# Kernel optimization log

Hardware: AMD Instinct MI355X
Metric: run time of the kernel (lower is better)

## Reference

```python
import jax, jax.numpy as jnp
import numpy as np
import math

H = 128
HEADS = 2
NEG = -float(1 << 32)
BN_EPS = 1e-5
LN_EPS = 1e-5


def _bn_eval(x, g, b):
    # BatchNorm1d in eval mode with running_mean=0, running_var=1
    return g * (x / jnp.sqrt(1.0 + BN_EPS)) + b


def _ln(x, g, b):
    mu = x.mean(-1, keepdims=True)
    var = ((x - mu) ** 2).mean(-1, keepdims=True)
    return g * (x - mu) / jnp.sqrt(var + LN_EPS) + b


def _multi_embed(tables, idx):
    # tables [F,V,H], idx [N,F] -> sum_f tables[f, idx[:,f]]  (ogb Atom/BondEncoder)
    F = tables.shape[0]
    return tables[jnp.arange(F)[None, :], idx].sum(axis=1)


def _gin_graph(x, edge_attr, edge_index, batch, num_graphs, atom_emb, bond_emb, eps, w1, b1, g1, be1, w2, b2, g2, be2):
    h = _multi_embed(atom_emb, x)  # [N,H]
    tgt, src = edge_index[0], edge_index[1]
    L = eps.shape[0]
    for l in range(L):
        e = _multi_embed(bond_emb[l], edge_attr)  # [E,H]
        msg = jax.nn.relu(h[src] + e)
        agg = jax.ops.segment_sum(msg, tgt, num_segments=h.shape[0])
        z = (1.0 + eps[l]) * h + agg
        z = jax.nn.relu(_bn_eval(z @ w1[l] + b1[l], g1[l], be1[l])) @ w2[l] + b2[l]
        h = _bn_eval(z, g2[l], be2[l])
        if l != L - 1:
            h = jax.nn.relu(h)  # dropout is identity in eval mode
    s = jax.ops.segment_sum(h, batch, num_segments=num_graphs)
    c = jax.ops.segment_sum(jnp.ones_like(h), batch, num_segments=num_graphs)
    return s / (c + 1e-9)  # mean pooling per graph


def _sab(X, wq, bq, wk, bk, wv, bv, wo, bo, l1g, l1b, l2g, l2b):
    # MAB(X, X) with HEADS heads, use_ln=True. X: [B,S,H]
    B, S, _ = X.shape
    dh = H // HEADS

    def split(T):  # torch split(last)+cat(dim0): head-major [HEADS*B, S, dh]
        return T.reshape(B, S, HEADS, dh).transpose(2, 0, 1, 3).reshape(HEADS * B, S, dh)

    Qs, Ks, Vs = split(X @ wq + bq), split(X @ wk + bk), split(X @ wv + bv)
    A = jax.nn.softmax(jnp.einsum('bqd,bkd->bqk', Qs, Ks) / math.sqrt(dh), axis=-1)
    O = Qs + jnp.einsum('bqk,bkd->bqd', A, Vs)
    O = O.reshape(HEADS, B, S, dh).transpose(1, 2, 0, 3).reshape(B, S, H)
    O = _ln(O, l1g, l1b)
    O = _ln(O @ wo + bo, l2g, l2b)
    return O


def setup_inputs() -> dict:
    key = jax.random.key(0)
    ks = iter(jax.random.split(key, 64))
    nk = lambda: next(ks)
    V, L = 64, 4
    NS, ES = 60000, 140000
    NM, EM = 150000, 350000
    S, M, D, B = 492, 600, 200, 64
    f32 = jnp.float32
    w = lambda *shp: jax.random.normal(nk(), shp, f32) * 0.05
    inp = {}
    inp['atom_emb'] = w(2, 9, V, H)
    inp['bond_emb'] = w(2, L, 3, V, H)
    inp['gin_eps'] = jnp.zeros((2, L), f32)
    inp['gin_w1'] = w(2, L, H, 2 * H); inp['gin_b1'] = jnp.zeros((2, L, 2 * H), f32)
    inp['gin_bn1_g'] = jnp.ones((2, L, 2 * H), f32); inp['gin_bn1_b'] = jnp.zeros((2, L, 2 * H), f32)
    inp['gin_w2'] = w(2, L, 2 * H, H); inp['gin_b2'] = jnp.zeros((2, L, H), f32)
    inp['gin_bn2_g'] = jnp.ones((2, L, H), f32); inp['gin_bn2_b'] = jnp.zeros((2, L, H), f32)
    for nm in ['sab_wq', 'sab_wk', 'sab_wv', 'sab_wo']:
        inp[nm] = w(H, H)
    for nm in ['sab_bq', 'sab_bk', 'sab_bv', 'sab_bo', 'sab_ln1_b', 'sab_ln2_b']:
        inp[nm] = jnp.zeros((H,), f32)
    inp['sab_ln1_g'] = jnp.ones((H,), f32); inp['sab_ln2_g'] = jnp.ones((H,), f32)
    inp['agg_wq'] = w(H, H); inp['agg_bq'] = jnp.zeros((H,), f32)
    inp['agg_wk'] = w(H, H); inp['agg_bk'] = jnp.zeros((H,), f32)
    inp['score_w1'] = w(H, H // 2); inp['score_b1'] = jnp.zeros((H // 2,), f32)
    inp['score_w2'] = w(H // 2, 1); inp['score_b2'] = jnp.zeros((1,), f32)
    inp['patient_emb'] = jax.random.uniform(nk(), (B, S), f32)
    inp['average_projection'] = jax.random.uniform(nk(), (D, M), f32) / M
    inp['sub_x'] = jax.random.randint(nk(), (NS, 9), 0, V)
    inp['sub_edge_attr'] = jax.random.randint(nk(), (ES, 3), 0, V)
    inp['sub_edge_index'] = jax.random.randint(nk(), (2, ES), 0, NS)
    inp['sub_batch'] = jax.random.randint(nk(), (NS,), 0, S)
    inp['mol_x'] = jax.random.randint(nk(), (NM, 9), 0, V)
    inp['mol_edge_attr'] = jax.random.randint(nk(), (EM, 3), 0, V)
    inp['mol_edge_index'] = jax.random.randint(nk(), (2, EM), 0, NM)
    inp['mol_batch'] = jax.random.randint(nk(), (NM,), 0, M)
    mask = jax.random.bernoulli(nk(), 0.3, (D, S))
    inp['mask'] = mask.at[:, 0].set(False)
    inp['num_sub'] = S
    inp['num_mol'] = M
    return inp


def reference(atom_emb, bond_emb, gin_eps, gin_w1, gin_b1, gin_bn1_g, gin_bn1_b, gin_w2, gin_b2, gin_bn2_g, gin_bn2_b, sab_wq, sab_bq, sab_wk, sab_bk, sab_wv, sab_bv, sab_wo, sab_bo, sab_ln1_g, sab_ln1_b, sab_ln2_g, sab_ln2_b, agg_wq, agg_bq, agg_wk, agg_bk, score_w1, score_b1, score_w2, score_b2, patient_emb, average_projection, sub_x, sub_edge_attr, sub_edge_index, sub_batch, mol_x, mol_edge_attr, mol_edge_index, mol_batch, mask, num_sub, num_mol):
    # substructure encoder (GINGraph #0) + SAB interaction
    sub = _gin_graph(sub_x, sub_edge_attr, sub_edge_index, sub_batch, num_sub, atom_emb[0], bond_emb[0], gin_eps[0], gin_w1[0], gin_b1[0], gin_bn1_g[0], gin_bn1_b[0], gin_w2[0], gin_b2[0], gin_bn2_g[0], gin_bn2_b[0])
    sub = _sab(sub[None], sab_wq, sab_bq, sab_wk, sab_bk, sab_wv, sab_bv, sab_wo, sab_bo, sab_ln1_g, sab_ln1_b, sab_ln2_g, sab_ln2_b)[0]  # [S,H]
    # molecule encoder (GINGraph #1) + drug-level averaging
    mol = _gin_graph(mol_x, mol_edge_attr, mol_edge_index, mol_batch, num_mol, atom_emb[1], bond_emb[1], gin_eps[1], gin_w1[1], gin_b1[1], gin_bn1_g[1], gin_bn1_b[1], gin_w2[1], gin_b2[1], gin_bn2_g[1], gin_bn2_b[1])
    mol_emb = average_projection @ mol  # [D,H]
    # AttnAgg: masked attention, per-patient reweighting via diag(fix_feat)
    Q = mol_emb @ agg_wq + agg_bq
    K = sub @ agg_wk + agg_bk
    attn = (Q @ K.T) / math.sqrt(H)
    attn = jax.nn.softmax(jnp.where(mask, NEG, attn), axis=-1)  # [D,S]
    agg = jnp.einsum('ds,bs,sh->bdh', attn, patient_emb, sub)  # [B,D,H]
    logits = (jax.nn.relu(agg @ score_w1 + score_b1) @ score_w2 + score_b2)[..., 0]
    return jax.nn.sigmoid(logits)  # y_prob [B,D]
```

## Files before the change

### kernel.cpp

```cpp
#include <hip/hip_runtime.h>


typedef short short8 __attribute__((ext_vector_type(8)));
typedef unsigned short us8 __attribute__((ext_vector_type(8)));
typedef float f32x4 __attribute__((ext_vector_type(4)));
typedef unsigned short us4 __attribute__((ext_vector_type(4)));

#define BN_RSQ 0.9999950000374997f
#define LN_EPS 1e-5f
#define NEGBIG -4294967296.0f

__device__ __forceinline__ unsigned short f2bf(float x) {
  union { float f; unsigned int u; } v; v.f = x;
  unsigned int r = v.u + 0x7fffu + ((v.u >> 16) & 1u);
  return (unsigned short)(r >> 16);
}
__device__ __forceinline__ float bf2f(unsigned short x) {
  union { unsigned int u; float f; } v; v.u = ((unsigned int)x) << 16;
  return v.f;
}

__global__ void prep_weights(const float* __restrict__ w1, const float* __restrict__ w2,
                             unsigned short* __restrict__ w1t, unsigned short* __restrict__ w2t) {
  int i = blockIdx.x * 256 + threadIdx.x;
  if (i >= 262144) return;
  int gl = i >> 15;
  int k1 = (i >> 8) & 127, c1 = i & 255;
  w1t[(gl << 15) + c1 * 128 + k1] = f2bf(w1[i]);
  int k2 = (i >> 7) & 255, c2 = i & 127;
  w2t[(gl << 15) + c2 * 256 + k2] = f2bf(w2[i]);
}

__global__ void prep_bond(const float* __restrict__ in, unsigned short* __restrict__ out, int n) {
  int i = blockIdx.x * 256 + threadIdx.x;
  if (i < n) out[i] = f2bf(in[i]);
}

__global__ __launch_bounds__(256) void mask_detect(const unsigned char* __restrict__ m,
                                                   int* __restrict__ flags, int nbytes) {
  __shared__ int lf[2];
  if (threadIdx.x == 0) { lf[0] = 0; lf[1] = 0; }
  __syncthreads();
  int f0 = 0, f1 = 0;
  for (int i = blockIdx.x * 256 + threadIdx.x; i < nbytes; i += gridDim.x * 256) {
    if (m[i]) { if ((i & 3) == 0) f0 = 1; else f1 = 1; }
  }
  if (f0) atomicOr(&lf[0], 1);
  if (f1) atomicOr(&lf[1], 1);
  __syncthreads();
  if (threadIdx.x == 0) {
    if (lf[0]) atomicOr(flags, 1);
    if (lf[1]) atomicOr(flags + 1, 1);
  }
}

__global__ void build_count(const int* __restrict__ ei_m, int Em,
                            const int* __restrict__ ei_s, int Es,
                            const int* __restrict__ bm, int Nm,
                            const int* __restrict__ bs, int Ns,
                            int* __restrict__ deg_e, int* __restrict__ deg_n,
                            int M, int NmR) {
  int i = blockIdx.x * 256 + threadIdx.x;
  if (i < Em) { atomicAdd(&deg_e[ei_m[i]], 1); return; }
  i -= Em;
  if (i < Es) { atomicAdd(&deg_e[NmR + ei_s[i]], 1); return; }
  i -= Es;
  if (i < Nm) { atomicAdd(&deg_n[bm[i]], 1); return; }
  i -= Nm;
  if (i < Ns) { atomicAdd(&deg_n[M + bs[i]], 1); }
}

__global__ __launch_bounds__(256) void scan_block(const int* __restrict__ cnt, int n,
                                                  int* __restrict__ excl, int* __restrict__ bsum) {
  int gid = blockIdx.x * 256 + threadIdx.x;
  int lane = threadIdx.x & 63, w = threadIdx.x >> 6;
  int v = (gid < n) ? cnt[gid] : 0;
  int x = v;
#pragma unroll
  for (int off = 1; off < 64; off <<= 1) {
    int y = __shfl_up(x, off, 64);
    if (lane >= off) x += y;
  }
  __shared__ int wt[4];
  if (lane == 63) wt[w] = x;
  __syncthreads();
  int add = 0;
  for (int i = 0; i < w; i++) add += wt[i];
  x += add;
  if (gid < n) excl[gid] = x - v;
  if (threadIdx.x == 255) bsum[blockIdx.x] = x;
}

__global__ __launch_bounds__(1024) void scan_top(int* __restrict__ bsum, int n) {
  int t = threadIdx.x;
  int lane = t & 63, w = t >> 6;
  int v = (t < n) ? bsum[t] : 0;
  int x = v;
#pragma unroll
  for (int off = 1; off < 64; off <<= 1) {
    int y = __shfl_up(x, off, 64);
    if (lane >= off) x += y;
  }
  __shared__ int wt[16];
  if (lane == 63) wt[w] = x;
  __syncthreads();
  int add = 0;
  for (int i = 0; i < w; i++) add += wt[i];
  x += add;
  if (t < n) bsum[t] = x - v;
}

__global__ void finalize_rowptr(const int* __restrict__ excl, const int* __restrict__ bsum,
                                int n, int total, int* __restrict__ rowptr) {
  int i = blockIdx.x * 256 + threadIdx.x;
  if (i < n) rowptr[i] = excl[i] + bsum[i >> 8];
  if (i == n) rowptr[n] = total;
}

__global__ void scatter_edges(const int* __restrict__ ei_m, const int* __restrict__ ea_m, int Em,
                              const int* __restrict__ ei_s, const int* __restrict__ ea_s, int Es, int NmR,
                              const int* __restrict__ rowptr_e,
                              int* __restrict__ cur_e, int4* __restrict__ epool) {
  int i = blockIdx.x * 256 + threadIdx.x;
  int g, src, a0, a1, a2;
  if (i < Em) {
    g = ei_m[i]; src = ei_m[Em + i];
    a0 = ea_m[i * 3]; a1 = ea_m[i * 3 + 1]; a2 = ea_m[i * 3 + 2];
  } else {
    int j = i - Em; if (j >= Es) return;
    g = NmR + ei_s[j]; src = NmR + ei_s[Es + j];
    a0 = ea_s[j * 3]; a1 = ea_s[j * 3 + 1]; a2 = ea_s[j * 3 + 2];
  }
  int slot = rowptr_e[g] + atomicAdd(&cur_e[g], 1);
  int p0 = a0 * 128, p1 = (64 + a1) * 128, p2 = (128 + a2) * 128;
  epool[slot] = make_int4(src * 128, 0, p0 | (p1 << 16), p2);
}

__global__ void scatter_nodes(const int* __restrict__ bm, int Nm,
                              const int* __restrict__ bs, int Ns, int M, int NmR,
                              const int* __restrict__ rowptr_n,
                              int* __restrict__ cur_n, int* __restrict__ npool) {
  int i = blockIdx.x * 256 + threadIdx.x;
  int g, node;
  if (i < Nm) { g = bm[i]; node = i; }
  else { int j = i - Nm; if (j >= Ns) return; g = M + bs[j]; node = NmR + j; }
  int slot = rowptr_n[g] + atomicAdd(&cur_n[g], 1);
  npool[slot] = node;
}

__global__ void embed_nodes(const int* __restrict__ x, const float* __restrict__ table,
                            unsigned short* __restrict__ h, int N) {
  int i = blockIdx.x * 256 + threadIdx.x;
  if (i >= N * 128) return;
  int n = i >> 7, c = i & 127;
  float s = 0.f;
#pragma unroll
  for (int f = 0; f < 9; f++) {
    int v = x[n * 9 + f];
    s += table[(f * 64 + v) * 128 + c];
  }
  h[i] = f2bf(s);
}

__global__ __launch_bounds__(256, 4) void gin_fused3(
    const unsigned short* __restrict__ hin, unsigned short* __restrict__ hout,
    const float* __restrict__ eps_all, int l, int NmR,
    const unsigned short* __restrict__ bt16,
    const int4* __restrict__ epool, const int* __restrict__ rowptr_e,
    const unsigned short* __restrict__ w1t_a, const float* __restrict__ b1_a,
    const float* __restrict__ g1_a, const float* __restrict__ be1_a,
    const unsigned short* __restrict__ w2t_a, const float* __restrict__ b2_a,
    const float* __restrict__ g2_a, const float* __restrict__ be2_a) {
  __shared__ __align__(16) unsigned char smem[38144];
  unsigned short* z1s = (unsigned short*)smem;
  unsigned short* zs  = (unsigned short*)(smem + 20736);
  int t = threadIdx.x;
  int r0 = blockIdx.x * 64;
  int g = (r0 < NmR) ? 1 : 0;
  int gl = g * 4 + l;
  const unsigned short* bt = bt16 + (size_t)gl * 3 * 64 * 128;
  const unsigned short* w1t = w1t_a + (size_t)gl * 32768;
  const unsigned short* w2t = w2t_a + (size_t)gl * 32768;
  const float* b1 = b1_a + gl * 256;
  const float* g1 = g1_a + gl * 256;
  const float* be1 = be1_a + gl * 256;
  const float* b2 = b2_a + gl * 128;
  const float* g2 = g2_a + gl * 128;
  const float* be2 = be2_a + gl * 128;
  float eps1 = 1.0f + eps_all[gl];
  int do_relu = (l != 3);

#pragma unroll
  for (int p = 0; p < 2; p++) {
    int lr = p * 32 + (t >> 3);
    int n = r0 + lr;
    int cb = (t & 7) * 16;
    float acc[16];
    {
      const unsigned short* hr = hin + (size_t)n * 128 + cb;
      us8 v0 = *(const us8*)hr, v1 = *(const us8*)(hr + 8);
#pragma unroll
      for (int k = 0; k < 8; k++) {
        acc[k]     = eps1 * bf2f(v0[k]);
        acc[8 + k] = eps1 * bf2f(v1[k]);
      }
    }
    int e0 = rowptr_e[n], e1 = rowptr_e[n + 1];
    for (int e = e0; e < e1; e++) {
      int4 rec = epool[e];
      const unsigned short* hs = hin + rec.x + cb;
      const unsigned short* q0 = bt + (rec.z & 0xffff) + cb;
      const unsigned short* q1 = bt + (((unsigned)rec.z) >> 16) + cb;
      const unsigned short* q2 = bt + rec.w + cb;
      us8 a0 = *(const us8*)hs, a1 = *(const us8*)(hs + 8);
      us8 b0 = *(const us8*)q0, b1v = *(const us8*)(q0 + 8);
      us8 c0 = *(const us8*)q1, c1 = *(const us8*)(q1 + 8);
      us8 d0 = *(const us8*)q2, d1 = *(const us8*)(q2 + 8);
#pragma unroll
      for (int k = 0; k < 8; k++) {
        acc[k]     += fmaxf(bf2f(a0[k]) + bf2f(b0[k]) + bf2f(c0[k]) + bf2f(d0[k]), 0.f);
        acc[8 + k] += fmaxf(bf2f(a1[k]) + bf2f(b1v[k]) + bf2f(c1[k]) + bf2f(d1[k]), 0.f);
      }
    }
    unsigned short ob[16];
#pragma unroll
    for (int k = 0; k < 16; k++) ob[k] = f2bf(acc[k]);
    unsigned short* zr = zs + lr * 136 + cb;
    *(us8*)zr = *(const us8*)&ob[0];
    *(us8*)(zr + 8) = *(const us8*)&ob[8];
  }
  __syncthreads();

  int lane = t & 63, wave = t >> 6;
  int quad = lane >> 4, l16 = lane & 15;
  {
    short8 bw[4][4];
    int cb = wave * 64;
#pragma unroll
    for (int nt = 0; nt < 4; nt++) {
      const unsigned short* p = w1t + (cb + nt * 16 + l16) * 128 + quad * 8;
#pragma unroll
      for (int kc = 0; kc < 4; kc++) bw[nt][kc] = *(const short8*)(p + kc * 32);
    }
    for (int mt = 0; mt < 4; mt++) {
      short8 af[4];
      const unsigned short* zrow = zs + (mt * 16 + l16) * 136 + quad * 8;
#pragma unroll
      for (int kc = 0; kc < 4; kc++)
        af[kc] = *(const short8*)(zrow + kc * 32);
#pragma unroll
      for (int nt = 0; nt < 4; nt++) {
        f32x4 acc = {0.f, 0.f, 0.f, 0.f};
#pragma unroll
        for (int kc = 0; kc < 4; kc++)
          acc = __builtin_amdgcn_mfma_f32_16x16x32_bf16(af[kc], bw[nt][kc], acc, 0, 0, 0);
        int c = cb + nt * 16 + l16;
        float sc = g1[c] * BN_RSQ, sh = be1[c], bb = b1[c];
#pragma unroll
        for (int reg = 0; reg < 4; reg++) {
          int r = mt * 16 + quad * 4 + reg;
          float y = (acc[reg] + bb) * sc + sh;
          z1s[r * 264 + c] = f2bf(fmaxf(y, 0.f));
        }
      }
      __syncthreads();
    }
  }
  {
    short8 bw[2][8];
    int cb = wave * 32;
#pragma unroll
    for (int nt = 0; nt < 2; nt++) {
      const unsigned short* p = w2t + (cb + nt * 16 + l16) * 256 + quad * 8;
#pragma unroll
      for (int kc = 0; kc < 8; kc++) bw[nt][kc] = *(const short8*)(p + kc * 32);
    }
    for (int mt = 0; mt < 4; mt++) {
      short8 af[8];
      const unsigned short* zrow = z1s + (mt * 16 + l16) * 264 + quad * 8;
#pragma unroll
      for (int kc = 0; kc < 8; kc++)
        af[kc] = *(const short8*)(zrow + kc * 32);
      __syncthreads();
#pragma unroll
      for (int nt = 0; nt < 2; nt++) {
        f32x4 acc = {0.f, 0.f, 0.f, 0.f};
#pragma unroll
        for (int kc = 0; kc < 8; kc++)
          acc = __builtin_amdgcn_mfma_f32_16x16x32_bf16(af[kc], bw[nt][kc], acc, 0, 0, 0);
        int c = cb + nt * 16 + l16;
        float sc = g2[c] * BN_RSQ, sh = be2[c], bb = b2[c];
#pragma unroll
        for (int reg = 0; reg < 4; reg++) {
          int r = mt * 16 + quad * 4 + reg;
          float y = (acc[reg] + bb) * sc + sh;
          if (do_relu) y = fmaxf(y, 0.f);
          z1s[r * 264 + c] = f2bf(y);
        }
      }
    }
  }
  __syncthreads();
  for (int i = t; i < 1024; i += 256) {
    int r = i >> 4, c8 = (i & 15) * 8;
    us8 v = *(const us8*)(z1s + r * 264 + c8);
    *(us8*)(hout + (size_t)(r0 + r) * 128 + c8) = v;
  }
}

__global__ __launch_bounds__(128) void pool_csr(const unsigned short* __restrict__ h,
                                                const int* __restrict__ npool,
                                                const int* __restrict__ rowptr_n,
                                                float* __restrict__ pooled, int nseg) {
  int m = blockIdx.x;
  if (m >= nseg) return;
  int st = rowptr_n[m];
  int e = rowptr_n[m + 1];
  int len = e - st;
  int c = threadIdx.x;
  float s = 0.f;
  int i = st;
  for (; i + 3 < e; i += 4) {
    int n0 = npool[i], n1 = npool[i + 1], n2 = npool[i + 2], n3 = npool[i + 3];
    float v0 = bf2f(h[(size_t)n0 * 128 + c]);
    float v1 = bf2f(h[(size_t)n1 * 128 + c]);
    float v2 = bf2f(h[(size_t)n2 * 128 + c]);
    float v3 = bf2f(h[(size_t)n3 * 128 + c]);
    s += (v0 + v1) + (v2 + v3);
  }
  for (; i < e; i++) s += bf2f(h[(size_t)npool[i] * 128 + c]);
  pooled[m * 128 + c] = s / ((float)len + 1e-9f);
}

__global__ __launch_bounds__(256) void gemm_tile(const float* __restrict__ A, const float* __restrict__ W,
                                                 const float* __restrict__ bias, float* __restrict__ C,
                                                 int K) {
  __shared__ float As[608];
  __shared__ float red[128];
  int r = blockIdx.x;
  int t = threadIdx.x;
  for (int i = t; i < K; i += 256) As[i] = A[(size_t)r * K + i];
  __syncthreads();
  int c = t & 127, half = t >> 7;
  int Kh = K >> 1;
  int k0 = half * Kh, k1 = k0 + Kh;
  float acc = 0.f;
#pragma unroll 8
  for (int k = k0; k < k1; k++) acc = fmaf(As[k], W[(size_t)k * 128 + c], acc);
  if (half) red[c] = acc;
  __syncthreads();
  if (!half) {
    float v = acc + red[c] + (bias ? bias[c] : 0.f);
    C[(size_t)r * 128 + c] = v;
  }
}

__global__ __launch_bounds__(256) void gemm_qkv(const float* __restrict__ A,
                                                const float* __restrict__ W0, const float* __restrict__ bi0, float* __restrict__ C0,
                                                const float* __restrict__ W1, const float* __restrict__ bi1, float* __restrict__ C1,
                                                const float* __restrict__ W2, const float* __restrict__ bi2, float* __restrict__ C2) {
  __shared__ float As[128];
  __shared__ float red[128];
  int r = blockIdx.x, which = blockIdx.y;
  const float* W = (which == 0) ? W0 : (which == 1) ? W1 : W2;
  const float* bias = (which == 0) ? bi0 : (which == 1) ? bi1 : bi2;
  float* C = (which == 0) ? C0 : (which == 1) ? C1 : C2;
  int t = threadIdx.x;
  if (t < 128) As[t] = A[(size_t)r * 128 + t];
  __syncthreads();
  int c = t & 127, half = t >> 7;
  int k0 = half * 64, k1 = k0 + 64;
  float acc = 0.f;
#pragma unroll 8
  for (int k = k0; k < k1; k++) acc = fmaf(As[k], W[(size_t)k * 128 + c], acc);
  if (half) red[c] = acc;
  __syncthreads();
  if (!half) C[(size_t)r * 128 + c] = acc + red[c] + bias[c];
}

__global__ __launch_bounds__(256) void sab_attn(const float* __restrict__ Q, const float* __restrict__ K,
                                                const float* __restrict__ V, float* __restrict__ O, int S) {
  int q = blockIdx.x, hd = blockIdx.y;
  int t = threadIdx.x;
  __shared__ float sc[512];
  __shared__ float red[8];
  __shared__ float pacc[4][64];
  const float* qrow = Q + q * 128 + hd * 64;
  for (int k = t; k < 512; k += 256) {
    float d = -1e30f;
    if (k < S) {
      const float* krow = K + k * 128 + hd * 64;
      d = 0.f;
#pragma unroll
      for (int j = 0; j < 64; j += 4) {
        float4 a = *(const float4*)(qrow + j);
        float4 b = *(const float4*)(krow + j);
        d += a.x * b.x + a.y * b.y + a.z * b.z + a.w * b.w;
      }
      d *= 0.125f;
    }
    sc[k] = d;
  }
  __syncthreads();
  float m = fmaxf(sc[t], sc[t + 256]);
  for (int off = 32; off; off >>= 1) m = fmaxf(m, __shfl_down(m, off));
  if ((t & 63) == 0) red[t >> 6] = m;
  __syncthreads();
  m = fmaxf(fmaxf(red[0], red[1]), fmaxf(red[2], red[3]));
  float p0 = __expf(sc[t] - m), p1 = __expf(sc[t + 256] - m);
  sc[t] = p0; sc[t + 256] = p1;
  float s = p0 + p1;
  for (int off = 32; off; off >>= 1) s += __shfl_down(s, off);
  if ((t & 63) == 0) red[4 + (t >> 6)] = s;
  __syncthreads();
  float inv = 1.f / (red[4] + red[5] + red[6] + red[7]);
  int d = t & 63, part = t >> 6;
  float acc = 0.f;
  for (int k = part; k < S; k += 4) acc += sc[k] * V[k * 128 + hd * 64 + d];
  pacc[part][d] = acc;
  __syncthreads();
  if (part == 0) {
    float o = (pacc[0][d] + pacc[1][d] + pacc[2][d] + pacc[3][d]) * inv;
    O[q * 128 + hd * 64 + d] = qrow[d] + o;
  }
}

__global__ __launch_bounds__(128) void ln_rows(const float* __restrict__ in, float* __restrict__ out,
                                               const float* __restrict__ g, const float* __restrict__ b) {
  int r = blockIdx.x, t = threadIdx.x;
  __shared__ float red[4];
  float x = in[r * 128 + t];
  float s = x;
  for (int off = 32; off; off >>= 1) s += __shfl_down(s, off);
  if ((t & 63) == 0) red[t >> 6] = s;
  __syncthreads();
  float mu = (red[0] + red[1]) * (1.f / 128.f);
  float dd = x - mu;
  float v = dd * dd;
  for (int off = 32; off; off >>= 1) v += __shfl_down(v, off);
  if ((t & 63) == 0) red[2 + (t >> 6)] = v;
  __syncthreads();
  float var = (red[2] + red[3]) * (1.f / 128.f);
  out[r * 128 + t] = g[t] * dd * rsqrtf(var + LN_EPS) + b[t];
}

__global__ __launch_bounds__(256) void agg_attn(const float* __restrict__ Q, const float* __restrict__ Kt,
                                                const void* __restrict__ mask, const int* __restrict__ flags,
                                                float* __restrict__ attn, int D, int S) {
  int d = blockIdx.x, t = threadIdx.x;
  __shared__ float sc[512];
  __shared__ float red[8];
  int layout = (flags[1] == 0) ? 0 : (flags[0] ? 1 : 2);
  const float* qrow = Q + d * 128;
  for (int s = t; s < 512; s += 256) {
    float v = NEGBIG;
    if (s < S) {
      int mi = d * S + s;
      bool msk;
      if (layout == 0)      msk = ((const int*)mask)[mi] != 0;
      else if (layout == 1) msk = ((const unsigned char*)mask)[mi] != 0;
      else                  msk = ((const float*)mask)[mi] != 0.f;
      if (!msk) {
        float dd = 0.f;
        const float* krow = Kt + s * 128;
#pragma unroll
        for (int j = 0; j < 128; j += 4) {
          float4 a = *(const float4*)(qrow + j);
          float4 b = *(const float4*)(krow + j);
          dd += a.x * b.x + a.y * b.y + a.z * b.z + a.w * b.w;
        }
        v = dd * 0.08838834764831845f;
      }
    }
    sc[s] = v;
  }
  __syncthreads();
  float m = fmaxf(sc[t], sc[t + 256]);
  for (int off = 32; off; off >>= 1) m = fmaxf(m, __shfl_down(m, off));
  if ((t & 63) == 0) red[t >> 6] = m;
  __syncthreads();
  m = fmaxf(fmaxf(red[0], red[1]), fmaxf(red[2], red[3]));
  float p0 = __expf(sc[t] - m), p1 = __expf(sc[t + 256] - m);
  float s2 = p0 + p1;
  for (int off = 32; off; off >>= 1) s2 += __shfl_down(s2, off);
  if ((t & 63) == 0) red[4 + (t >> 6)] = s2;
  __syncthreads();
  float inv = 1.f / (red[4] + red[5] + red[6] + red[7]);
  attn[d * S + t] = p0 * inv;
  if (t + 256 < S) attn[d * S + t + 256] = p1 * inv;
}

__global__ void prep_subT(const float* __restrict__ subf, unsigned short* __restrict__ subT, int S) {
  int i = blockIdx.x * 256 + threadIdx.x;
  if (i >= 128 * 512) return;
  int hh = i >> 9, k = i & 511;
  subT[i] = (k < S) ? f2bf(subf[k * 128 + hh]) : (unsigned short)0;
}

__global__ __launch_bounds__(256) void agg_mfma(const float* __restrict__ attn, const float* __restrict__ pat,
                                                const unsigned short* __restrict__ subT,
                                                float* __restrict__ aggT, int D, int S) {
  int d = blockIdx.x, t = threadIdx.x;
  __shared__ unsigned short As[64][40];
  int lane = t & 63, wave = t >> 6;
  int quad = lane >> 4, l16 = lane & 15;
  f32x4 acc[8];
#pragma unroll
  for (int nt = 0; nt < 8; nt++) acc[nt] = (f32x4){0.f, 0.f, 0.f, 0.f};
  const float* arow = attn + d * S;
  int srow = t >> 2, skb = (t & 3) * 8;
  for (int c = 0; c < 16; c++) {
    int s0 = c * 32;
    __syncthreads();
    unsigned short v[8];
#pragma unroll
    for (int j = 0; j < 8; j++) {
      int s = s0 + skb + j;
      float x = (s < S) ? arow[s] * pat[srow * S + s] : 0.f;
      v[j] = f2bf(x);
    }
    *(us4*)&As[srow][skb]     = *(us4*)&v[0];
    *(us4*)&As[srow][skb + 4] = *(us4*)&v[4];
    __syncthreads();
    short8 af = *(const short8*)&As[16 * wave + l16][quad * 8];
#pragma unroll
    for (int nt = 0; nt < 8; nt++) {
      short8 bf = *(const short8*)(subT + (nt * 16 + l16) * 512 + s0 + quad * 8);
      acc[nt] = __builtin_amdgcn_mfma_f32_16x16x32_bf16(af, bf, acc[nt], 0, 0, 0);
    }
  }
#pragma unroll
  for (int nt = 0; nt < 8; nt++) {
    int hh = nt * 16 + l16;
#pragma unroll
    for (int reg = 0; reg < 4; reg++) {
      int b = 16 * wave + quad * 4 + reg;
      aggT[((size_t)(b * D + d)) * 128 + hh] = acc[nt][reg];
    }
  }
}

__global__ __launch_bounds__(256) void score_head(const float* __restrict__ aggT,
                                                  const float* __restrict__ w1, const float* __restrict__ b1,
                                                  const float* __restrict__ w2, const float* __restrict__ b2,
                                                  float* __restrict__ out, int total) {
  int i = blockIdx.x * 4 + (threadIdx.x >> 6);
  int j = threadIdx.x & 63;
  if (i >= total) return;
  const float* av = aggT + (size_t)i * 128;
  float acc = b1[j];
#pragma unroll 8
  for (int k = 0; k < 128; k++) acc = fmaf(av[k], w1[k * 64 + j], acc);
  acc = fmaxf(acc, 0.f) * w2[j];
  for (int off = 32; off; off >>= 1) acc += __shfl_down(acc, off);
  if (j == 0) {
    float x = acc + b2[0];
    out[i] = 1.f / (1.f + __expf(-x));
  }
}

extern "C" void kernel_launch(void* const* d_in, const int* in_sizes, int n_in,
                              void* d_out, int out_size, void* d_ws, size_t ws_size,
                              hipStream_t stream) {
  const float* atom_emb = (const float*)d_in[0];
  const float* bond_emb = (const float*)d_in[1];
  const float* gin_eps  = (const float*)d_in[2];
  const float* gin_w1   = (const float*)d_in[3];
  const float* gin_b1   = (const float*)d_in[4];
  const float* bn1g     = (const float*)d_in[5];
  const float* bn1b     = (const float*)d_in[6];
  const float* gin_w2   = (const float*)d_in[7];
  const float* gin_b2   = (const float*)d_in[8];
  const float* bn2g     = (const float*)d_in[9];
  const float* bn2b     = (const float*)d_in[10];
  const float* sab_wq = (const float*)d_in[11];
  const float* sab_wk = (const float*)d_in[12];
  const float* sab_wv = (const float*)d_in[13];
  const float* sab_wo = (const float*)d_in[14];
  const float* sab_bq = (const float*)d_in[15];
  const float* sab_bk = (const float*)d_in[16];
  const float* sab_bv = (const float*)d_in[17];
  const float* sab_bo = (const float*)d_in[18];
  const float* ln1b = (const float*)d_in[19];
  const float* ln2b = (const float*)d_in[20];
  const float* ln1g = (const float*)d_in[21];
  const float* ln2g = (const float*)d_in[22];
  const float* agg_wq = (const float*)d_in[23];
  const float* agg_bq = (const float*)d_in[24];
  const float* agg_wk = (const float*)d_in[25];
  const float* agg_bk = (const float*)d_in[26];
  const float* score_w1 = (const float*)d_in[27];
  const float* score_b1 = (const float*)d_in[28];
  const float* score_w2 = (const float*)d_in[29];
  const float* score_b2 = (const float*)d_in[30];
  const float* patient  = (const float*)d_in[31];
  const float* avgproj  = (const float*)d_in[32];
  const int* sub_x     = (const int*)d_in[33];
  const int* sub_ea    = (const int*)d_in[34];
  const int* sub_ei    = (const int*)d_in[35];
  const int* sub_batch = (const int*)d_in[36];
  const int* mol_x     = (const int*)d_in[37];
  const int* mol_ea    = (const int*)d_in[38];
  const int* mol_ei    = (const int*)d_in[39];
  const int* mol_batch = (const int*)d_in[40];
  const void* mask     = d_in[41];

  const int Ns = in_sizes[33] / 9, Es = in_sizes[34] / 3;
  const int Nm = in_sizes[37] / 9, Em = in_sizes[38] / 3;
  const int S = 492, M = 600, D = 200, B = 64;
  const int NmR = (Nm + 63) & ~63;
  const int NsR = (Ns + 63) & ~63;
  const int NTOT = NmR + NsR;
  const int NSEG = M + S;
  const int ETOT = Em + Es;
  const int BONDE = 2 * 4 * 3 * 64 * 128;

  char* Wp = (char*)d_ws;
  size_t off = 0;
  auto alloc = [&](size_t bytes) -> void* {
    void* p = Wp + off;
    off = (off + bytes + 255) & ~(size_t)255;
    return p;
  };
  unsigned short* h0 = (unsigned short*)alloc((size_t)NTOT * 128 * 2);
  unsigned short* h1 = (unsigned short*)alloc((size_t)NTOT * 128 * 2);
  unsigned short* w1t = (unsigned short*)alloc(262144 * 2);
  unsigned short* w2t = (unsigned short*)alloc(262144 * 2);
  unsigned short* bt16 = (unsigned short*)alloc((size_t)BONDE * 2);
  int4* epool  = (int4*)alloc((size_t)ETOT * 16);
  int*  npool  = (int*)alloc((size_t)(Nm + Ns) * 4);
  int*  excl_e = (int*)alloc((size_t)NTOT * 4);
  int*  bsum_e = (int*)alloc(1024 * 4);
  int*  excl_n = (int*)alloc((size_t)NSEG * 4);
  int*  bsum_n = (int*)alloc(1024 * 4);
  int*  rowptr_e = (int*)alloc((size_t)(NTOT + 1) * 4);
  int*  rowptr_n = (int*)alloc((size_t)(NSEG + 1) * 4);
  char* zstart = Wp + off;
  int*  deg_e  = (int*)alloc((size_t)NTOT * 4);
  int*  deg_n  = (int*)alloc((size_t)NSEG * 4);
  int*  cur_e  = (int*)alloc((size_t)NTOT * 4);
  int*  cur_n  = (int*)alloc((size_t)NSEG * 4);
  int*  flags  = (int*)alloc(8);
  size_t zsize = (size_t)((Wp + off) - zstart);
  float* pooled_all = (float*)alloc((size_t)NSEG * 128 * 4);
  float* pooled_mol = pooled_all;
  float* pooled_sub = pooled_all + (size_t)M * 128;
  float* Qb   = (float*)alloc((size_t)S * 128 * 4);
  float* Kb   = (float*)alloc((size_t)S * 128 * 4);
  float* Vb   = (float*)alloc((size_t)S * 128 * 4);
  float* Ob   = (float*)alloc((size_t)S * 128 * 4);
  float* O2b  = (float*)alloc((size_t)S * 128 * 4);
  float* subf = (float*)alloc((size_t)S * 128 * 4);
  unsigned short* subT = (unsigned short*)alloc((size_t)128 * 512 * 2);
  float* mol_embb = (float*)alloc((size_t)D * 128 * 4);
  float* aggQb = (float*)alloc((size_t)D * 128 * 4);
  float* aggKb = (float*)alloc((size_t)S * 128 * 4);
  float* attnb = (float*)alloc((size_t)D * S * 4);
  float* aggTb = (float*)alloc((size_t)B * D * 128 * 4);
  (void)ws_size; (void)n_in; (void)out_size;

  hipMemsetAsync(zstart, 0, zsize, stream);
  prep_weights<<<1024, 256, 0, stream>>>(gin_w1, gin_w2, w1t, w2t);
  prep_bond<<<(BONDE + 255) / 256, 256, 0, stream>>>(bond_emb, bt16, BONDE);
  mask_detect<<<64, 256, 0, stream>>>((const unsigned char*)mask, flags, D * S);

  int total_cnt = Em + Es + Nm + Ns;
  build_count<<<(total_cnt + 255) / 256, 256, 0, stream>>>(
      mol_ei, Em, sub_ei, Es, mol_batch, Nm, sub_batch, Ns, deg_e, deg_n, M, NmR);
  int nb_e = (NTOT + 255) / 256;
  int nb_n = (NSEG + 255) / 256;
  scan_block<<<nb_e, 256, 0, stream>>>(deg_e, NTOT, excl_e, bsum_e);
  scan_top<<<1, 1024, 0, stream>>>(bsum_e, nb_e);
  scan_block<<<nb_n, 256, 0, stream>>>(deg_n, NSEG, excl_n, bsum_n);
  scan_top<<<1, 1024, 0, stream>>>(bsum_n, nb_n);
  finalize_rowptr<<<(NTOT + 256) / 256 + 1, 256, 0, stream>>>(excl_e, bsum_e, NTOT, ETOT, rowptr_e);
  finalize_rowptr<<<(NSEG + 256) / 256 + 1, 256, 0, stream>>>(excl_n, bsum_n, NSEG, Nm + Ns, rowptr_n);
  scatter_edges<<<(ETOT + 255) / 256, 256, 0, stream>>>(
      mol_ei, mol_ea, Em, sub_ei, sub_ea, Es, NmR, rowptr_e, cur_e, epool);
  scatter_nodes<<<(Nm + Ns + 255) / 256, 256, 0, stream>>>(
      mol_batch, Nm, sub_batch, Ns, M, NmR, rowptr_n, cur_n, npool);

  embed_nodes<<<(Nm * 128 + 255) / 256, 256, 0, stream>>>(
      mol_x, atom_emb + (size_t)1 * 9 * 64 * 128, h0, Nm);
  embed_nodes<<<(Ns * 128 + 255) / 256, 256, 0, stream>>>(
      sub_x, atom_emb + (size_t)0 * 9 * 64 * 128, h0 + (size_t)NmR * 128, Ns);
  unsigned short* hin = h0; unsigned short* hout = h1;
  for (int l = 0; l < 4; l++) {
    gin_fused3<<<NTOT / 64, 256, 0, stream>>>(
        hin, hout, gin_eps, l, NmR, bt16, epool, rowptr_e,
        w1t, gin_b1, bn1g, bn1b, w2t, gin_b2, bn2g, bn2b);
    unsigned short* tmp = hin; hin = hout; hout = tmp;
  }
  pool_csr<<<NSEG, 128, 0, stream>>>(hin, npool, rowptr_n, pooled_all, NSEG);

  gemm_qkv<<<dim3(S, 3), 256, 0, stream>>>(pooled_sub,
                                           sab_wq, sab_bq, Qb,
                                           sab_wk, sab_bk, Kb,
                                           sab_wv, sab_bv, Vb);
  sab_attn<<<dim3(S, 2), 256, 0, stream>>>(Qb, Kb, Vb, Ob, S);
  ln_rows<<<S, 128, 0, stream>>>(Ob, Ob, ln1g, ln1b);
  gemm_tile<<<S, 256, 0, stream>>>(Ob, sab_wo, sab_bo, O2b, 128);
  ln_rows<<<S, 128, 0, stream>>>(O2b, subf, ln2g, ln2b);
  prep_subT<<<(128 * 512 + 255) / 256, 256, 0, stream>>>(subf, subT, S);

  gemm_tile<<<D, 256, 0, stream>>>(avgproj, pooled_mol, (const float*)nullptr, mol_embb, 600);

  gemm_tile<<<D, 256, 0, stream>>>(mol_embb, agg_wq, agg_bq, aggQb, 128);
  gemm_tile<<<S, 256, 0, stream>>>(subf, agg_wk, agg_bk, aggKb, 128);
  agg_attn<<<D, 256, 0, stream>>>(aggQb, aggKb, mask, flags, attnb, D, S);
  agg_mfma<<<D, 256, 0, stream>>>(attnb, patient, subT, aggTb, D, S);
  score_head<<<(B * D + 3) / 4, 256, 0, stream>>>(aggTb, score_w1, score_b1, score_w2, score_b2,
                                                  (float*)d_out, B * D);
}
```

Before: 1.045 ms.

## Merge small preprocessing kernels and fuse Wo GEMM with LayerNorm

Several small setup launches are merged into combined kernels: weight, bond and mask prep, the two prefix scans, the row-pointer finalisation, the edge and node scatters, the two embeddings, and the two attention Q/K projections. The Wo projection is fused with the second LayerNorm, which removes an intermediate buffer. The GIN aggregation loop also unpacks bf16 pairs straight from 32-bit words instead of per-element conversion. The goal is less launch overhead and fewer global round trips, at the cost of branchier combined kernels.

```diff
diff --git a/kernel.cpp b/kernel.cpp
--- a/kernel.cpp
+++ b/kernel.cpp
@@ -5,6 +5,7 @@
 typedef unsigned short us8 __attribute__((ext_vector_type(8)));
 typedef float f32x4 __attribute__((ext_vector_type(4)));
 typedef unsigned short us4 __attribute__((ext_vector_type(4)));
+typedef unsigned int u32;
 
 #define BN_RSQ 0.9999950000374997f
 #define LN_EPS 1e-5f
@@ -20,29 +21,31 @@
   return v.f;
 }
 
-__global__ void prep_weights(const float* __restrict__ w1, const float* __restrict__ w2,
-                             unsigned short* __restrict__ w1t, unsigned short* __restrict__ w2t) {
-  int i = blockIdx.x * 256 + threadIdx.x;
-  if (i >= 262144) return;
-  int gl = i >> 15;
-  int k1 = (i >> 8) & 127, c1 = i & 255;
-  w1t[(gl << 15) + c1 * 128 + k1] = f2bf(w1[i]);
-  int k2 = (i >> 7) & 255, c2 = i & 127;
-  w2t[(gl << 15) + c2 * 256 + k2] = f2bf(w2[i]);
-}
-
-__global__ void prep_bond(const float* __restrict__ in, unsigned short* __restrict__ out, int n) {
-  int i = blockIdx.x * 256 + threadIdx.x;
-  if (i < n) out[i] = f2bf(in[i]);
-}
-
-__global__ __launch_bounds__(256) void mask_detect(const unsigned char* __restrict__ m,
-                                                   int* __restrict__ flags, int nbytes) {
+__global__ __launch_bounds__(256) void prep_all(
+    const float* __restrict__ w1, const float* __restrict__ w2,
+    unsigned short* __restrict__ w1t, unsigned short* __restrict__ w2t,
+    const float* __restrict__ bond, unsigned short* __restrict__ bt16, int bonde,
+    const unsigned char* __restrict__ m, int* __restrict__ flags, int maskn) {
   __shared__ int lf[2];
+  int b = blockIdx.x;
+  if (b < 1024) {
+    int i = b * 256 + threadIdx.x;
+    int gl = i >> 15;
+    int k1 = (i >> 8) & 127, c1 = i & 255;
+    w1t[(gl << 15) + c1 * 128 + k1] = f2bf(w1[i]);
+    int k2 = (i >> 7) & 255, c2 = i & 127;
+    w2t[(gl << 15) + c2 * 256 + k2] = f2bf(w2[i]);
+    return;
+  }
+  if (b < 1792) {
+    int i = (b - 1024) * 256 + threadIdx.x;
+    if (i < bonde) bt16[i] = f2bf(bond[i]);
+    return;
+  }
   if (threadIdx.x == 0) { lf[0] = 0; lf[1] = 0; }
   __syncthreads();
   int f0 = 0, f1 = 0;
-  for (int i = blockIdx.x * 256 + threadIdx.x; i < nbytes; i += gridDim.x * 256) {
+  for (int i = (b - 1792) * 256 + threadIdx.x; i < maskn; i += 64 * 256) {
     if (m[i]) { if ((i & 3) == 0) f0 = 1; else f1 = 1; }
   }
   if (f0) atomicOr(&lf[0], 1);
@@ -70,9 +73,13 @@
   if (i < Ns) { atomicAdd(&deg_n[M + bs[i]], 1); }
 }
 
-__global__ __launch_bounds__(256) void scan_block(const int* __restrict__ cnt, int n,
-                                                  int* __restrict__ excl, int* __restrict__ bsum) {
-  int gid = blockIdx.x * 256 + threadIdx.x;
+__global__ __launch_bounds__(256) void scan_block2(
+    const int* __restrict__ cntE, int nE, int* __restrict__ exclE, int* __restrict__ bsumE, int nbE,
+    const int* __restrict__ cntN, int nN, int* __restrict__ exclN, int* __restrict__ bsumN) {
+  const int* cnt; int n; int* excl; int* bsum; int blk;
+  if (blockIdx.x < (unsigned)nbE) { cnt = cntE; n = nE; excl = exclE; bsum = bsumE; blk = blockIdx.x; }
+  else { cnt = cntN; n = nN; excl = exclN; bsum = bsumN; blk = blockIdx.x - nbE; }
+  int gid = blk * 256 + threadIdx.x;
   int lane = threadIdx.x & 63, w = threadIdx.x >> 6;
   int v = (gid < n) ? cnt[gid] : 0;
   int x = v;
@@ -88,10 +95,13 @@
   for (int i = 0; i < w; i++) add += wt[i];
   x += add;
   if (gid < n) excl[gid] = x - v;
-  if (threadIdx.x == 255) bsum[blockIdx.x] = x;
-}
-
-__global__ __launch_bounds__(1024) void scan_top(int* __restrict__ bsum, int n) {
+  if (threadIdx.x == 255) bsum[blk] = x;
+}
+
+__global__ __launch_bounds__(1024) void scan_top2(int* __restrict__ bsumE, int nE,
+                                                  int* __restrict__ bsumN, int nN) {
+  int* bsum = blockIdx.x ? bsumN : bsumE;
+  int n = blockIdx.x ? nN : nE;
   int t = threadIdx.x;
   int lane = t & 63, w = t >> 6;
   int v = (t < n) ? bsum[t] : 0;
@@ -110,56 +120,71 @@
   if (t < n) bsum[t] = x - v;
 }
 
-__global__ void finalize_rowptr(const int* __restrict__ excl, const int* __restrict__ bsum,
-                                int n, int total, int* __restrict__ rowptr) {
+__global__ void finalize2(const int* __restrict__ exclE, const int* __restrict__ bsumE,
+                          int nE, int totE, int* __restrict__ rowE,
+                          const int* __restrict__ exclN, const int* __restrict__ bsumN,
+                          int nN, int totN, int* __restrict__ rowN) {
   int i = blockIdx.x * 256 + threadIdx.x;
-  if (i < n) rowptr[i] = excl[i] + bsum[i >> 8];
-  if (i == n) rowptr[n] = total;
-}
-
-__global__ void scatter_edges(const int* __restrict__ ei_m, const int* __restrict__ ea_m, int Em,
-                              const int* __restrict__ ei_s, const int* __restrict__ ea_s, int Es, int NmR,
-                              const int* __restrict__ rowptr_e,
-                              int* __restrict__ cur_e, int4* __restrict__ epool) {
+  if (i <= nE) {
+    rowE[i] = (i < nE) ? (exclE[i] + bsumE[i >> 8]) : totE;
+    return;
+  }
+  int j = i - nE - 1;
+  if (j <= nN) rowN[j] = (j < nN) ? (exclN[j] + bsumN[j >> 8]) : totN;
+}
+
+__global__ void scatter2(const int* __restrict__ ei_m, const int* __restrict__ ea_m, int Em,
+                         const int* __restrict__ ei_s, const int* __restrict__ ea_s, int Es, int NmR,
+                         const int* __restrict__ rowptr_e, int* __restrict__ cur_e,
+                         int4* __restrict__ epool,
+                         const int* __restrict__ bm, int Nm,
+                         const int* __restrict__ bs, int Ns, int M,
+                         const int* __restrict__ rowptr_n, int* __restrict__ cur_n,
+                         int* __restrict__ npool) {
   int i = blockIdx.x * 256 + threadIdx.x;
-  int g, src, a0, a1, a2;
-  if (i < Em) {
-    g = ei_m[i]; src = ei_m[Em + i];
-    a0 = ea_m[i * 3]; a1 = ea_m[i * 3 + 1]; a2 = ea_m[i * 3 + 2];
-  } else {
-    int j = i - Em; if (j >= Es) return;
-    g = NmR + ei_s[j]; src = NmR + ei_s[Es + j];
-    a0 = ea_s[j * 3]; a1 = ea_s[j * 3 + 1]; a2 = ea_s[j * 3 + 2];
-  }
-  int slot = rowptr_e[g] + atomicAdd(&cur_e[g], 1);
-  int p0 = a0 * 128, p1 = (64 + a1) * 128, p2 = (128 + a2) * 128;
-  epool[slot] = make_int4(src * 128, 0, p0 | (p1 << 16), p2);
-}
-
-__global__ void scatter_nodes(const int* __restrict__ bm, int Nm,
-                              const int* __restrict__ bs, int Ns, int M, int NmR,
-                              const int* __restrict__ rowptr_n,
-                              int* __restrict__ cur_n, int* __restrict__ npool) {
-  int i = blockIdx.x * 256 + threadIdx.x;
+  if (i < Em + Es) {
+    int g, src, a0, a1, a2;
+    if (i < Em) {
+      g = ei_m[i]; src = ei_m[Em + i];
+      a0 = ea_m[i * 3]; a1 = ea_m[i * 3 + 1]; a2 = ea_m[i * 3 + 2];
+    } else {
+      int j = i - Em;
+      g = NmR + ei_s[j]; src = NmR + ei_s[Es + j];
+      a0 = ea_s[j * 3]; a1 = ea_s[j * 3 + 1]; a2 = ea_s[j * 3 + 2];
+    }
+    int slot = rowptr_e[g] + atomicAdd(&cur_e[g], 1);
+    int p0 = a0 * 128, p1 = (64 + a1) * 128, p2 = (128 + a2) * 128;
+    epool[slot] = make_int4(src * 128, 0, p0 | (p1 << 16), p2);
+    return;
+  }
+  int k = i - (Em + Es);
+  if (k >= Nm + Ns) return;
   int g, node;
-  if (i < Nm) { g = bm[i]; node = i; }
-  else { int j = i - Nm; if (j >= Ns) return; g = M + bs[j]; node = NmR + j; }
+  if (k < Nm) { g = bm[k]; node = k; }
+  else { int j = k - Nm; g = M + bs[j]; node = NmR + j; }
   int slot = rowptr_n[g] + atomicAdd(&cur_n[g], 1);
   npool[slot] = node;
 }
 
-__global__ void embed_nodes(const int* __restrict__ x, const float* __restrict__ table,
-                            unsigned short* __restrict__ h, int N) {
+__global__ void embed2(const int* __restrict__ xm, const int* __restrict__ xs,
+                       const float* __restrict__ atab, int Nm, int Ns, int NmR,
+                       unsigned short* __restrict__ h) {
   int i = blockIdx.x * 256 + threadIdx.x;
-  if (i >= N * 128) return;
-  int n = i >> 7, c = i & 127;
+  const int* x; const float* table; int n, c, outn;
+  if (i < Nm * 128) {
+    n = i >> 7; c = i & 127; x = xm; table = atab + (size_t)9 * 64 * 128; outn = n;
+  } else {
+    int j = i - Nm * 128;
+    if (j >= Ns * 128) return;
+    n = j >> 7; c = j & 127; x = xs; table = atab; outn = NmR + n;
+  }
   float s = 0.f;
 #pragma unroll
   for (int f = 0; f < 9; f++) {
     int v = x[n * 9 + f];
     s += table[(f * 64 + v) * 128 + c];
   }
-  h[i] = f2bf(s);
+  h[(size_t)outn * 128 + c] = f2bf(s);
 }
 
 __global__ __launch_bounds__(256, 4) void gin_fused3(
@@ -195,39 +220,50 @@
     int lr = p * 32 + (t >> 3);
     int n = r0 + lr;
     int cb = (t & 7) * 16;
-    float acc[16];
+    float lo[8], hi[8];
     {
-      const unsigned short* hr = hin + (size_t)n * 128 + cb;
-      us8 v0 = *(const us8*)hr, v1 = *(const us8*)(hr + 8);
-#pragma unroll
-      for (int k = 0; k < 8; k++) {
-        acc[k]     = eps1 * bf2f(v0[k]);
-        acc[8 + k] = eps1 * bf2f(v1[k]);
+      const u32* hr = (const u32*)(hin + (size_t)n * 128 + cb);
+      uint4 h0v = *(const uint4*)hr;
+      uint4 h1v = *(const uint4*)(hr + 4);
+      u32 hd[8] = {h0v.x, h0v.y, h0v.z, h0v.w, h1v.x, h1v.y, h1v.z, h1v.w};
+#pragma unroll
+      for (int j = 0; j < 8; j++) {
+        lo[j] = eps1 * __uint_as_float(hd[j] << 16);
+        hi[j] = eps1 * __uint_as_float(hd[j] & 0xffff0000u);
       }
     }
     int e0 = rowptr_e[n], e1 = rowptr_e[n + 1];
     for (int e = e0; e < e1; e++) {
       int4 rec = epool[e];
-      const unsigned short* hs = hin + rec.x + cb;
-      const unsigned short* q0 = bt + (rec.z & 0xffff) + cb;
-      const unsigned short* q1 = bt + (((unsigned)rec.z) >> 16) + cb;
-      const unsigned short* q2 = bt + rec.w + cb;
-      us8 a0 = *(const us8*)hs, a1 = *(const us8*)(hs + 8);
-      us8 b0 = *(const us8*)q0, b1v = *(const us8*)(q0 + 8);
-      us8 c0 = *(const us8*)q1, c1 = *(const us8*)(q1 + 8);
-      us8 d0 = *(const us8*)q2, d1 = *(const us8*)(q2 + 8);
-#pragma unroll
-      for (int k = 0; k < 8; k++) {
-        acc[k]     += fmaxf(bf2f(a0[k]) + bf2f(b0[k]) + bf2f(c0[k]) + bf2f(d0[k]), 0.f);
-        acc[8 + k] += fmaxf(bf2f(a1[k]) + bf2f(b1v[k]) + bf2f(c1[k]) + bf2f(d1[k]), 0.f);
+      const u32* hs = (const u32*)(hin + rec.x + cb);
+      const u32* q0 = (const u32*)(bt + (rec.z & 0xffff) + cb);
+      const u32* q1 = (const u32*)(bt + (((unsigned)rec.z) >> 16) + cb);
+      const u32* q2 = (const u32*)(bt + rec.w + cb);
+      uint4 A0 = *(const uint4*)hs, A1 = *(const uint4*)(hs + 4);
+      uint4 B0 = *(const uint4*)q0, B1 = *(const uint4*)(q0 + 4);
+      uint4 C0 = *(const uint4*)q1, C1 = *(const uint4*)(q1 + 4);
+      uint4 D0 = *(const uint4*)q2, D1 = *(const uint4*)(q2 + 4);
+      u32 ad[8] = {A0.x, A0.y, A0.z, A0.w, A1.x, A1.y, A1.z, A1.w};
+      u32 bd[8] = {B0.x, B0.y, B0.z, B0.w, B1.x, B1.y, B1.z, B1.w};
+      u32 cd[8] = {C0.x, C0.y, C0.z, C0.w, C1.x, C1.y, C1.z, C1.w};
+      u32 dd[8] = {D0.x, D0.y, D0.z, D0.w, D1.x, D1.y, D1.z, D1.w};
+#pragma unroll
+      for (int j = 0; j < 8; j++) {
+        float sl = __uint_as_float(ad[j] << 16) + __uint_as_float(bd[j] << 16)
+                 + __uint_as_float(cd[j] << 16) + __uint_as_float(dd[j] << 16);
+        float sh = __uint_as_float(ad[j] & 0xffff0000u) + __uint_as_float(bd[j] & 0xffff0000u)
+                 + __uint_as_float(cd[j] & 0xffff0000u) + __uint_as_float(dd[j] & 0xffff0000u);
+        lo[j] += fmaxf(sl, 0.f);
+        hi[j] += fmaxf(sh, 0.f);
       }
     }
-    unsigned short ob[16];
-#pragma unroll
-    for (int k = 0; k < 16; k++) ob[k] = f2bf(acc[k]);
-    unsigned short* zr = zs + lr * 136 + cb;
-    *(us8*)zr = *(const us8*)&ob[0];
-    *(us8*)(zr + 8) = *(const us8*)&ob[8];
+    u32 od[8];
+#pragma unroll
+    for (int j = 0; j < 8; j++)
+      od[j] = (u32)f2bf(lo[j]) | (((u32)f2bf(hi[j])) << 16);
+    u32* zr = (u32*)(zs + lr * 136 + cb);
+    *(uint4*)zr = make_uint4(od[0], od[1], od[2], od[3]);
+    *(uint4*)(zr + 4) = make_uint4(od[4], od[5], od[6], od[7]);
   }
   __syncthreads();
 
@@ -376,6 +412,73 @@
   if (half) red[c] = acc;
   __syncthreads();
   if (!half) C[(size_t)r * 128 + c] = acc + red[c] + bias[c];
+}
+
+__global__ __launch_bounds__(256) void gemm_aggqk(
+    const float* __restrict__ Aq, const float* __restrict__ Wq, const float* __restrict__ bq,
+    float* __restrict__ Cq, int D,
+    const float* __restrict__ Ak, const float* __restrict__ Wk, const float* __restrict__ bk,
+    float* __restrict__ Ck) {
+  __shared__ float As[128];
+  __shared__ float red[128];
+  int r = blockIdx.x;
+  const float* A; const float* W; const float* bias; float* C; int rr;
+  if (r < D) { A = Aq; W = Wq; bias = bq; C = Cq; rr = r; }
+  else { A = Ak; W = Wk; bias = bk; C = Ck; rr = r - D; }
+  int t = threadIdx.x;
+  if (t < 128) As[t] = A[(size_t)rr * 128 + t];
+  __syncthreads();
+  int c = t & 127, half = t >> 7;
+  int k0 = half * 64, k1 = k0 + 64;
+  float acc = 0.f;
+#pragma unroll 8
+  for (int k = k0; k < k1; k++) acc = fmaf(As[k], W[(size_t)k * 128 + c], acc);
+  if (half) red[c] = acc;
+  __syncthreads();
+  if (!half) C[(size_t)rr * 128 + c] = acc + red[c] + bias[c];
+}
+
+__global__ __launch_bounds__(256) void gemm_wo_ln(const float* __restrict__ A,
+                                                  const float* __restrict__ W, const float* __restrict__ bias,
+                                                  const float* __restrict__ lg, const float* __restrict__ lb,
+                                                  float* __restrict__ subf) {
+  __shared__ float As[128];
+  __shared__ float row[128];
+  __shared__ float red2[4];
+  int r = blockIdx.x;
+  int t = threadIdx.x;
+  if (t < 128) As[t] = A[(size_t)r * 128 + t];
+  __syncthreads();
+  int c = t & 127, half = t >> 7;
+  int k0 = half * 64, k1 = k0 + 64;
+  float acc = 0.f;
+#pragma unroll 8
+  for (int k = k0; k < k1; k++) acc = fmaf(As[k], W[(size_t)k * 128 + c], acc);
+  if (half) row[c] = acc;
+  __syncthreads();
+  if (!half) row[c] = acc + row[c] + bias[c];
+  __syncthreads();
+  if (t < 128) {
+    float x = row[t];
+    float s = x;
+    for (int off = 32; off; off >>= 1) s += __shfl_down(s, off);
+    if ((t & 63) == 0) red2[t >> 6] = s;
+  }
+  __syncthreads();
+  if (t < 128) {
+    float mu = (red2[0] + red2[1]) * (1.f / 128.f);
+    float dd = row[t] - mu;
+    float v = dd * dd;
+    for (int off = 32; off; off >>= 1) v += __shfl_down(v, off);
+    if ((t & 63) == 0) red2[2 + (t >> 6)] = v;
+  }
+  __syncthreads();
+  if (t < 128) {
+    float mu = (red2[0] + red2[1]) * (1.f / 128.f);
+    float var = (red2[2] + red2[3]) * (1.f / 128.f);
+    float dd = row[t] - mu;
+    subf[(size_t)r * 128 + t] = lg[t] * dd * rsqrtf(var + LN_EPS) + lb[t];
+  }
 }
 
 __global__ __launch_bounds__(256) void sab_attn(const float* __restrict__ Q, const float* __restrict__ K,
@@ -649,7 +752,6 @@
   float* Kb   = (float*)alloc((size_t)S * 128 * 4);
   float* Vb   = (float*)alloc((size_t)S * 128 * 4);
   float* Ob   = (float*)alloc((size_t)S * 128 * 4);
-  float* O2b  = (float*)alloc((size_t)S * 128 * 4);
   float* subf = (float*)alloc((size_t)S * 128 * 4);
   unsigned short* subT = (unsigned short*)alloc((size_t)128 * 512 * 2);
   float* mol_embb = (float*)alloc((size_t)D * 128 * 4);
@@ -660,30 +762,27 @@
   (void)ws_size; (void)n_in; (void)out_size;
 
   hipMemsetAsync(zstart, 0, zsize, stream);
-  prep_weights<<<1024, 256, 0, stream>>>(gin_w1, gin_w2, w1t, w2t);
-  prep_bond<<<(BONDE + 255) / 256, 256, 0, stream>>>(bond_emb, bt16, BONDE);
-  mask_detect<<<64, 256, 0, stream>>>((const unsigned char*)mask, flags, D * S);
+  prep_all<<<1856, 256, 0, stream>>>(gin_w1, gin_w2, w1t, w2t,
+                                     bond_emb, bt16, BONDE,
+                                     (const unsigned char*)mask, flags, D * S);
 
   int total_cnt = Em + Es + Nm + Ns;
   build_count<<<(total_cnt + 255) / 256, 256, 0, stream>>>(
       mol_ei, Em, sub_ei, Es, mol_batch, Nm, sub_batch, Ns, deg_e, deg_n, M, NmR);
   int nb_e = (NTOT + 255) / 256;
   int nb_n = (NSEG + 255) / 256;
-  scan_block<<<nb_e, 256, 0, stream>>>(deg_e, NTOT, excl_e, bsum_e);
-  scan_top<<<1, 1024, 0, stream>>>(bsum_e, nb_e);
-  scan_block<<<nb_n, 256, 0, stream>>>(deg_n, NSEG, excl_n, bsum_n);
-  scan_top<<<1, 1024, 0, stream>>>(bsum_n, nb_n);
-  finalize_rowptr<<<(NTOT + 256) / 256 + 1, 256, 0, stream>>>(excl_e, bsum_e, NTOT, ETOT, rowptr_e);
-  finalize_rowptr<<<(NSEG + 256) / 256 + 1, 256, 0, stream>>>(excl_n, bsum_n, NSEG, Nm + Ns, rowptr_n);
-  scatter_edges<<<(ETOT + 255) / 256, 256, 0, stream>>>(
-      mol_ei, mol_ea, Em, sub_ei, sub_ea, Es, NmR, rowptr_e, cur_e, epool);
-  scatter_nodes<<<(Nm + Ns + 255) / 256, 256, 0, stream>>>(
-      mol_batch, Nm, sub_batch, Ns, M, NmR, rowptr_n, cur_n, npool);
-
-  embed_nodes<<<(Nm * 128 + 255) / 256, 256, 0, stream>>>(
-      mol_x, atom_emb + (size_t)1 * 9 * 64 * 128, h0, Nm);
-  embed_nodes<<<(Ns * 128 + 255) / 256, 256, 0, stream>>>(
-      sub_x, atom_emb + (size_t)0 * 9 * 64 * 128, h0 + (size_t)NmR * 128, Ns);
+  scan_block2<<<nb_e + nb_n, 256, 0, stream>>>(deg_e, NTOT, excl_e, bsum_e, nb_e,
+                                               deg_n, NSEG, excl_n, bsum_n);
+  scan_top2<<<2, 1024, 0, stream>>>(bsum_e, nb_e, bsum_n, nb_n);
+  finalize2<<<((NTOT + 1) + (NSEG + 1) + 1 + 255) / 256, 256, 0, stream>>>(
+      excl_e, bsum_e, NTOT, ETOT, rowptr_e,
+      excl_n, bsum_n, NSEG, Nm + Ns, rowptr_n);
+  scatter2<<<(ETOT + Nm + Ns + 255) / 256, 256, 0, stream>>>(
+      mol_ei, mol_ea, Em, sub_ei, sub_ea, Es, NmR, rowptr_e, cur_e, epool,
+      mol_batch, Nm, sub_batch, Ns, M, rowptr_n, cur_n, npool);
+
+  embed2<<<((Nm + Ns) * 128 + 255) / 256, 256, 0, stream>>>(
+      mol_x, sub_x, atom_emb, Nm, Ns, NmR, h0);
   unsigned short* hin = h0; unsigned short* hout = h1;
   for (int l = 0; l < 4; l++) {
     gin_fused3<<<NTOT / 64, 256, 0, stream>>>(
@@ -699,14 +798,13 @@
                                            sab_wv, sab_bv, Vb);
   sab_attn<<<dim3(S, 2), 256, 0, stream>>>(Qb, Kb, Vb, Ob, S);
   ln_rows<<<S, 128, 0, stream>>>(Ob, Ob, ln1g, ln1b);
-  gemm_tile<<<S, 256, 0, stream>>>(Ob, sab_wo, sab_bo, O2b, 128);
-  ln_rows<<<S, 128, 0, stream>>>(O2b, subf, ln2g, ln2b);
+  gemm_wo_ln<<<S, 256, 0, stream>>>(Ob, sab_wo, sab_bo, ln2g, ln2b, subf);
   prep_subT<<<(128 * 512 + 255) / 256, 256, 0, stream>>>(subf, subT, S);
 
   gemm_tile<<<D, 256, 0, stream>>>(avgproj, pooled_mol, (const float*)nullptr, mol_embb, 600);
 
-  gemm_tile<<<D, 256, 0, stream>>>(mol_embb, agg_wq, agg_bq, aggQb, 128);
-  gemm_tile<<<S, 256, 0, stream>>>(subf, agg_wk, agg_bk, aggKb, 128);
+  gemm_aggqk<<<D + S, 256, 0, stream>>>(mol_embb, agg_wq, agg_bq, aggQb, D,
+                                        subf, agg_wk, agg_bk, aggKb);
   agg_attn<<<D, 256, 0, stream>>>(aggQb, aggKb, mask, flags, attnb, D, S);
   agg_mfma<<<D, 256, 0, stream>>>(attnb, patient, subT, aggTb, D, S);
   score_head<<<(B * D + 3) / 4, 256, 0, stream>>>(aggTb, score_w1, score_b1, score_w2, score_b2,
```

New measurement: 1.016 ms. -2.8%, faster.
